# Optimization experiments

Measured on AMD Instinct MI355X. Metric: run time of the kernel, lower is better.

The kernel has to match this reference:

```python
import jax, jax.numpy as jnp
import numpy as np

N_HEADS = 8

def setup_inputs() -> dict:
    key = jax.random.key(0)
    ks = jax.random.split(key, 12)
    B, S2, C, H, W = 2, 2048, 1280, 256, 256
    s = 0.02  # weight init scale
    return {
        'hidden_states': jax.random.normal(ks[0], (B, S2, C), dtype=jnp.float32),
        'src_mask': (jax.random.uniform(ks[1], (B, 1, H, W)) > 0.5).astype(jnp.float32),
        'attn_wq': jax.random.normal(ks[2], (C, C), dtype=jnp.float32) * s,
        'attn_wk': jax.random.normal(ks[3], (C, C), dtype=jnp.float32) * s,
        'attn_wv': jax.random.normal(ks[4], (C, C), dtype=jnp.float32) * s,
        'out_w': jax.random.normal(ks[5], (C, C), dtype=jnp.float32) * s,
        'out_b': jnp.zeros((C,), dtype=jnp.float32),
        'proc_wq': jax.random.normal(ks[6], (C, C), dtype=jnp.float32) * s,
        'proc_wk': jax.random.normal(ks[7], (C, C), dtype=jnp.float32) * s,
        'proc_wv': jax.random.normal(ks[8], (C, C), dtype=jnp.float32) * s,
        'ww': jax.random.normal(ks[9], (C + 1, 1), dtype=jnp.float32) * s,
        'wb': jnp.zeros((1,), dtype=jnp.float32),
    }


def reference(hidden_states, src_mask, attn_wq, attn_wk, attn_wv, out_w, out_b,
              proc_wq, proc_wk, proc_wv, ww, wb):
    B, S2, C = hidden_states.shape
    S = S2 // 2  # condition_flag=False: sequence is two images concatenated
    _, _, H, W = src_mask.shape
    r = int(np.sqrt((H * W) / S))  # nearest-neighbor downsample ratio
    # F.interpolate(mode='nearest') with exact integer ratio == strided slice
    m = src_mask[:, 0, ::r, ::r].reshape(B, S, 1)          # [B, S, 1]
    mask = jnp.concatenate([m, m], axis=1)                 # [B, 2S, 1]
    # sigmoid gate blending the two query projections
    gate_in = jnp.concatenate([hidden_states, mask], axis=-1)  # [B, 2S, C+1]
    w = jax.nn.sigmoid(gate_in @ ww + wb)                  # [B, 2S, 1]
    query = (hidden_states @ attn_wq) * w + (hidden_states @ proc_wq) * (1.0 - w)
    # keys/values: first half through attn's projections, second half through processor's
    e1, e2 = hidden_states[:, :S], hidden_states[:, S:]
    key = jnp.concatenate([e1 @ attn_wk, e2 @ proc_wk], axis=1)
    value = jnp.concatenate([e1 @ attn_wv, e2 @ proc_wv], axis=1)
    d = C // N_HEADS
    def split_heads(x):
        return x.reshape(B, S2, N_HEADS, d).transpose(0, 2, 1, 3)  # [B, H, S2, d]
    qh, kh, vh = split_heads(query), split_heads(key), split_heads(value)
    scale = float(1.0 / np.sqrt(d))
    scores = jnp.einsum('bhqd,bhkd->bhqk', qh, kh) * scale
    probs = jax.nn.softmax(scores, axis=-1)
    out = jnp.einsum('bhqk,bhkd->bhqd', probs, vh)
    out = out.transpose(0, 2, 1, 3).reshape(B, S2, C)
    out = out @ out_w + out_b
    # residual connection, rescale_output_factor == 1
    return out + hidden_states
```

## Files before the change

### kernel.cpp

```cpp
#include <hip/hip_runtime.h>

typedef unsigned short u16;
typedef u16 u16x4 __attribute__((ext_vector_type(4)));
typedef u16 u16x8 __attribute__((ext_vector_type(8)));
typedef __bf16 bf16x8 __attribute__((ext_vector_type(8)));
typedef float f32x4 __attribute__((ext_vector_type(4)));
typedef unsigned u32x4 __attribute__((ext_vector_type(4)));

#define DEVI __device__ __forceinline__

#if __has_builtin(__builtin_amdgcn_exp2f)
#define EXP2F __builtin_amdgcn_exp2f
#else
#define EXP2F exp2f
#endif

DEVI u16 f2b(float f) {
  unsigned u = __builtin_bit_cast(unsigned, f);
  u += 0x7fffu + ((u >> 16) & 1u);
  return (u16)(u >> 16);
}

DEVI float b2f(u16 v) { return __builtin_bit_cast(float, (unsigned)v << 16); }

DEVI unsigned cvtpk_bf16(float lo, float hi) {
  unsigned r;
  asm("v_cvt_pk_bf16_f32 %0, %1, %2" : "=v"(r) : "v"(lo), "v"(hi));
  return r;
}

DEVI f32x4 mfma16(u16x8 a, u16x8 b, f32x4 c) {
  return __builtin_amdgcn_mfma_f32_16x16x32_bf16(
      __builtin_bit_cast(bf16x8, a), __builtin_bit_cast(bf16x8, b), c, 0, 0, 0);
}

DEVI void async_copy16(const u16* g, u16* l) {
  __builtin_amdgcn_global_load_lds(
      (__attribute__((address_space(1))) unsigned int*)(g),
      (__attribute__((address_space(3))) unsigned int*)(l), 16, 0, 0);
}

DEVI void fence_barrier() {
  asm volatile("" ::: "memory");
  __builtin_amdgcn_s_barrier();
  asm volatile("" ::: "memory");
}

__global__ void prep_kernel(const float* __restrict__ hs, const float* __restrict__ mask,
                            const float* __restrict__ ww, const float* __restrict__ wb,
                            u16* __restrict__ hsb, float* __restrict__ wgate) {
  int token = blockIdx.x;
  int tid = threadIdx.x;
  const float* row = hs + (size_t)token * 1280;
  u16* orow = hsb + (size_t)token * 1280;
  float acc = 0.f;
#pragma unroll
  for (int i = 0; i < 5; i++) {
    int c = i * 256 + tid;
    float v = row[c];
    orow[c] = f2b(v);
    acc += v * ww[c];
  }
#pragma unroll
  for (int off = 1; off < 64; off <<= 1) acc += __shfl_xor(acc, off);
  __shared__ float partial[4];
  int wid = tid >> 6;
  if ((tid & 63) == 0) partial[wid] = acc;
  __syncthreads();
  if (tid == 0) {
    float tot = partial[0] + partial[1] + partial[2] + partial[3];
    int b = token >> 11, t = token & 2047;
    int s = t & 1023;
    float mv = mask[b * 65536 + ((s >> 5) * 8) * 256 + (s & 31) * 8];
    float z = tot + mv * ww[1280] + wb[0];
    wgate[token] = 1.f / (1.f + __expf(-z));
  }
}

__global__ void wtrans_kernel(const float* w0, const float* w1, const float* w2,
                              const float* w3, const float* w4, const float* w5,
                              const float* w6, u16* __restrict__ out) {
  const float* src;
  switch (blockIdx.z) {
    case 0: src = w0; break; case 1: src = w1; break; case 2: src = w2; break;
    case 3: src = w3; break; case 4: src = w4; break; case 5: src = w5; break;
    default: src = w6; break;
  }
  u16* dst = out + (size_t)blockIdx.z * 1280 * 1280;
  __shared__ float tile[32][33];
  int tx = threadIdx.x & 31, ty = threadIdx.x >> 5;
  int k0 = blockIdx.x * 32, n0 = blockIdx.y * 32;
#pragma unroll
  for (int r = 0; r < 4; r++)
    tile[ty + r * 8][tx] = src[(size_t)(k0 + ty + r * 8) * 1280 + n0 + tx];
  __syncthreads();
#pragma unroll
  for (int r = 0; r < 4; r++)
    dst[(size_t)(n0 + ty + r * 8) * 1280 + k0 + tx] = f2b(tile[tx][ty + r * 8]);
}

__launch_bounds__(256, 4)
__global__ void gemm_qdual_kernel(const u16* __restrict__ A, const u16* __restrict__ Wt,
                                  const float* __restrict__ wgate, float qscale,
                                  u16* __restrict__ Qout) {
  const int K = 1280, N = 1280;
  const size_t WSZ = (size_t)1280 * 1280;
  __shared__ u16 As[128 * 32];
  __shared__ u16 Bs[64 * 32];
  __shared__ u16 Bs2[64 * 32];

  int tid = threadIdx.x;
  int wid = tid >> 6, lane = tid & 63;
  int q = lane & 15, jl = lane >> 4;
  int nb = blockIdx.x, mb = blockIdx.y, z = blockIdx.z;
  int m0 = mb * 128, n0 = nb * 128;

  const u16* B0 = Wt + 0 * WSZ;
  const u16* B1 = Wt + 4 * WSZ;

  f32x4 zero = {0.f, 0.f, 0.f, 0.f};
  f32x4 acc[4][4];
#pragma unroll
  for (int i = 0; i < 4; i++)
#pragma unroll
    for (int j = 0; j < 4; j++) acc[i][j] = zero;

  int wr = wid >> 1, wc = wid & 1;
  int brow = tid >> 2, bseg = tid & 3;

  for (int kk = 0; kk < 40; kk++) {
    int k0 = kk * 32;
#pragma unroll
    for (int i = 0; i < 2; i++) {
      int slot = i * 256 + tid;
      int row = slot >> 2, seg = slot & 3;
      async_copy16(A + (size_t)(m0 + row) * K + k0 + seg * 8, As + (size_t)(i * 256 + wid * 64) * 8);
    }
    int nrow = n0 + (z << 6) + brow;
    async_copy16(B0 + (size_t)nrow * K + k0 + bseg * 8, Bs + (size_t)tid * 8);
    async_copy16(B1 + (size_t)nrow * K + k0 + bseg * 8, Bs2 + (size_t)tid * 8);
    asm volatile("s_waitcnt vmcnt(0)" ::: "memory");
    __syncthreads();

    u16x8 af[4];
#pragma unroll
    for (int mi = 0; mi < 4; mi++)
      af[mi] = *(const u16x8*)(As + (wr * 64 + mi * 16 + q) * 32 + jl * 8);
#pragma unroll
    for (int ni = 0; ni < 2; ni++) {
      u16x8 bf0 = *(const u16x8*)(Bs + (wc * 32 + ni * 16 + q) * 32 + jl * 8);
      u16x8 bf1 = *(const u16x8*)(Bs2 + (wc * 32 + ni * 16 + q) * 32 + jl * 8);
#pragma unroll
      for (int mi = 0; mi < 4; mi++) {
        acc[mi][ni] = mfma16(af[mi], bf0, acc[mi][ni]);
        acc[mi][2 + ni] = mfma16(af[mi], bf1, acc[mi][2 + ni]);
      }
    }
    __syncthreads();
  }

#pragma unroll
  for (int mi = 0; mi < 4; mi++)
#pragma unroll
    for (int r = 0; r < 4; r++) {
      int row = m0 + wr * 64 + mi * 16 + (jl << 2) + r;
      float w = wgate[row];
#pragma unroll
      for (int ni = 0; ni < 2; ni++) {
        int col = n0 + (z << 6) + wc * 32 + ni * 16 + q;
        float v = (w * acc[mi][ni][r] + (1.f - w) * acc[mi][2 + ni][r]) * qscale;
        Qout[(size_t)row * N + col] = f2b(v);
      }
    }
}

__launch_bounds__(256, 4)
__global__ void gemm_kv_kernel(const u16* __restrict__ A, const u16* __restrict__ Wt,
                               u16* __restrict__ Kout, u16* __restrict__ VTout) {
  const int K = 1280, N = 1280;
  const size_t WSZ = (size_t)1280 * 1280;
  __shared__ u16 As[128 * 32];
  __shared__ u16 Bs[64 * 32];
  __shared__ u16 Bs2[64 * 32];

  int tid = threadIdx.x;
  int wid = tid >> 6, lane = tid & 63;
  int q = lane & 15, jl = lane >> 4;
  int nb = blockIdx.x, mb = blockIdx.y;
  bool isV = (blockIdx.z == 1);
  int m0 = mb * 128, n0 = nb * 128;
  bool first = ((m0 & 2047) < 1024);

  const u16* B0 = isV ? (first ? Wt + 2 * WSZ : Wt + 6 * WSZ)
                      : (first ? Wt + 1 * WSZ : Wt + 5 * WSZ);

  f32x4 zero = {0.f, 0.f, 0.f, 0.f};
  f32x4 acc[4][4];
#pragma unroll
  for (int i = 0; i < 4; i++)
#pragma unroll
    for (int j = 0; j < 4; j++) acc[i][j] = zero;

  int wr = wid >> 1, wc = wid & 1;
  int brow = tid >> 2, bseg = tid & 3;

  for (int kk = 0; kk < 40; kk++) {
    int k0 = kk * 32;
#pragma unroll
    for (int i = 0; i < 2; i++) {
      int slot = i * 256 + tid;
      int row = slot >> 2, seg = slot & 3;
      async_copy16(A + (size_t)(m0 + row) * K + k0 + seg * 8, As + (size_t)(i * 256 + wid * 64) * 8);
    }
    async_copy16(B0 + (size_t)(n0 + brow) * K + k0 + bseg * 8, Bs + (size_t)tid * 8);
    async_copy16(B0 + (size_t)(n0 + 64 + brow) * K + k0 + bseg * 8, Bs2 + (size_t)tid * 8);
    asm volatile("s_waitcnt vmcnt(0)" ::: "memory");
    __syncthreads();

    u16x8 af[4];
#pragma unroll
    for (int mi = 0; mi < 4; mi++)
      af[mi] = *(const u16x8*)(As + (wr * 64 + mi * 16 + q) * 32 + jl * 8);
    const u16* Bsel = wc ? Bs2 : Bs;
    u16x8 bfr[4];
#pragma unroll
    for (int ni = 0; ni < 4; ni++)
      bfr[ni] = *(const u16x8*)(Bsel + (ni * 16 + q) * 32 + jl * 8);
#pragma unroll
    for (int mi = 0; mi < 4; mi++)
#pragma unroll
      for (int ni = 0; ni < 4; ni++)
        acc[mi][ni] = mfma16(af[mi], bfr[ni], acc[mi][ni]);
    __syncthreads();
  }

  if (!isV) {
#pragma unroll
    for (int mi = 0; mi < 4; mi++)
#pragma unroll
      for (int ni = 0; ni < 4; ni++)
#pragma unroll
        for (int r = 0; r < 4; r++) {
          int row = m0 + wr * 64 + mi * 16 + (jl << 2) + r;
          int col = n0 + wc * 64 + ni * 16 + q;
          Kout[(size_t)row * N + col] = f2b(acc[mi][ni][r]);
        }
  } else {
#pragma unroll
    for (int mi = 0; mi < 4; mi++)
#pragma unroll
      for (int ni = 0; ni < 4; ni++) {
        int row0 = m0 + wr * 64 + mi * 16 + (jl << 2);
        int col = n0 + wc * 64 + ni * 16 + q;
        int b = row0 >> 11, s = row0 & 2047;
        int h = col / 160, c_in = col - h * 160;
        u16x4 v = {f2b(acc[mi][ni][0]), f2b(acc[mi][ni][1]),
                   f2b(acc[mi][ni][2]), f2b(acc[mi][ni][3])};
        *(u16x4*)(VTout + ((size_t)(b * 8 + h) * 160 + c_in) * 2048 + s) = v;
      }
  }
}

template <int SPLIT>
__launch_bounds__(256)
__global__ void flash_kernel(const u16* __restrict__ Q, const u16* __restrict__ Kg,
                             const u16* __restrict__ VTg, u16* __restrict__ O,
                             u16* __restrict__ Opart, float* __restrict__ MLbuf) {
  const int C = 1280;
  int bid = blockIdx.x;
  int qb = bid & 31, h = (bid >> 5) & 7, b = bid >> 8;
  int sp = (SPLIT > 1) ? (int)blockIdx.y : 0;
  int tid = threadIdx.x, wid = tid >> 6, lane = tid & 63;
  int q = lane & 15, jl = lane >> 4;

  int t0, NT;
  if (SPLIT == 3) { t0 = sp * 11; NT = (sp < 2) ? 11 : 10; }
  else if (SPLIT == 1) { t0 = 0; NT = 32; }
  else { t0 = sp * (32 / SPLIT); NT = 32 / SPLIT; }

  const size_t baseQ = ((size_t)(b * 2048 + qb * 64)) * C + h * 160;
  const size_t baseK = ((size_t)(b * 2048)) * C + h * 160;
  const size_t baseVT = (size_t)(b * 8 + h) * 160 * 2048;

  __shared__ u16 Ks[64 * 160];
  __shared__ u16 Vts[160 * 64];

  const u16* kbase = Kg + baseK + (size_t)(t0 * 64) * C;
  const u16* vbase = VTg + baseVT + t0 * 64;
  unsigned koff[5];
#pragma unroll
  for (int j = 0; j < 5; j++) {
    int s = (wid + 4 * j) * 64 + lane;
    int r = s / 20, cp = s - r * 20;
    int c = cp ^ ((r >> 1) & 3);
    koff[j] = (unsigned)(r * C + c * 8);
  }
  unsigned voff[5];
#pragma unroll
  for (int j = 0; j < 5; j++) {
    int gc = (wid + 4 * j) * 64 + lane;
    int c = gc >> 3, jj = gc & 7;
    voff[j] = (unsigned)(c * 2048 + ((jj ^ (c & 7)) << 3));
  }

#define STAGE_K()                                                  \
  do {                                                             \
    _Pragma("unroll") for (int j = 0; j < 5; j++)                  \
        async_copy16(kbase + koff[j], Ks + (wid + 4 * j) * 512);   \
  } while (0)
#define STAGE_V()                                                  \
  do {                                                             \
    _Pragma("unroll") for (int j = 0; j < 5; j++)                  \
        async_copy16(vbase + voff[j], Vts + (wid + 4 * j) * 512);  \
  } while (0)

  const int kro = ((jl ^ ((q >> 1) & 3)) << 3);

  const int addr0 = (q + 16 * ((jl * 2 + 0) & 3)) << 2;
  const int addr1 = (q + 16 * ((jl * 2 + 1) & 3)) << 2;
  const bool hihalf = (lane >= 32);

  u16x8 qf[5];
  {
    const u16* qrow = Q + baseQ + (size_t)(wid * 16 + q) * C;
#pragma unroll
    for (int ks = 0; ks < 5; ks++)
      qf[ks] = *(const u16x8*)(qrow + ks * 32 + jl * 8);
  }

  f32x4 zero = {0.f, 0.f, 0.f, 0.f};
  f32x4 oacc[10];
#pragma unroll
  for (int i = 0; i < 10; i++) oacc[i] = zero;
  float mrow = -1e30f, lrow = 0.f;

  STAGE_K();
  STAGE_V();

  for (int kti = 0; kti < NT; kti++) {
    bool last = (kti == NT - 1);
    asm volatile("s_waitcnt vmcnt(5)" ::: "memory");
    fence_barrier();

    f32x4 sc[4];
#pragma unroll
    for (int ct = 0; ct < 4; ct++) {
      f32x4 a = zero;
#pragma unroll
      for (int ks = 0; ks < 5; ks++) {
        u16x8 kf = *(const u16x8*)(&Ks[(ct * 16 + q) * 160 + ks * 32 + kro]);
        a = mfma16(kf, qf[ks], a);
      }
      sc[ct] = a;
    }

    fence_barrier();
    if (!last) { kbase += 64 * C; STAGE_K(); }

    float m = sc[0][0];
#pragma unroll
    for (int ct = 0; ct < 4; ct++)
#pragma unroll
      for (int r = 0; r < 4; r++) m = fmaxf(m, sc[ct][r]);
    m = fmaxf(m, __shfl_xor(m, 16));
    m = fmaxf(m, __shfl_xor(m, 32));

    if (__any(m > mrow + 8.f)) {
      float mnew = fmaxf(mrow, m);
      float alpha = EXP2F(mrow - mnew);
      mrow = mnew;
      float rs = 0.f;
#pragma unroll
      for (int ct = 0; ct < 4; ct++)
#pragma unroll
        for (int r = 0; r < 4; r++) {
          float p = EXP2F(sc[ct][r] - mnew);
          sc[ct][r] = p;
          rs += p;
        }
      lrow = lrow * alpha + rs;
#pragma unroll
      for (int ci = 0; ci < 10; ci++) oacc[ci] *= alpha;
    } else {
      float rs = 0.f;
#pragma unroll
      for (int ct = 0; ct < 4; ct++)
#pragma unroll
        for (int r = 0; r < 4; r++) {
          float p = EXP2F(sc[ct][r] - mrow);
          sc[ct][r] = p;
          rs += p;
        }
      lrow += rs;
    }

    unsigned pk0[4], pk1[4];
#pragma unroll
    for (int ct = 0; ct < 4; ct++) {
      pk0[ct] = cvtpk_bf16(sc[ct][0], sc[ct][1]);
      pk1[ct] = cvtpk_bf16(sc[ct][2], sc[ct][3]);
    }

    if (!last) { asm volatile("s_waitcnt vmcnt(5)" ::: "memory"); }
    else       { asm volatile("s_waitcnt vmcnt(0)" ::: "memory"); }
    fence_barrier();

#pragma unroll
    for (int kt2 = 0; kt2 < 2; kt2++) {
      const int cA = kt2 * 2, cB = kt2 * 2 + 1;
      int a0 = __builtin_amdgcn_ds_bpermute(addr0, (int)pk0[cA]);
      int a1 = __builtin_amdgcn_ds_bpermute(addr0, (int)pk1[cA]);
      int a2 = __builtin_amdgcn_ds_bpermute(addr1, (int)pk0[cA]);
      int a3 = __builtin_amdgcn_ds_bpermute(addr1, (int)pk1[cA]);
      int b0 = __builtin_amdgcn_ds_bpermute(addr0, (int)pk0[cB]);
      int b1 = __builtin_amdgcn_ds_bpermute(addr0, (int)pk1[cB]);
      int b2 = __builtin_amdgcn_ds_bpermute(addr1, (int)pk0[cB]);
      int b3 = __builtin_amdgcn_ds_bpermute(addr1, (int)pk1[cB]);
      u32x4 d;
      d[0] = (unsigned)(hihalf ? b0 : a0);
      d[1] = (unsigned)(hihalf ? b1 : a1);
      d[2] = (unsigned)(hihalf ? b2 : a2);
      d[3] = (unsigned)(hihalf ? b3 : a3);
      u16x8 pf = __builtin_bit_cast(u16x8, d);
#pragma unroll
      for (int ci = 0; ci < 10; ci++) {
        int c = ci * 16 + q;
        int jj = kt2 * 4 + jl;
        u16x8 vf = *(const u16x8*)(&Vts[c * 64 + ((jj ^ (c & 7)) << 3)]);
        oacc[ci] = mfma16(vf, pf, oacc[ci]);
      }
    }

    fence_barrier();
    if (!last) { vbase += 64; STAGE_V(); }
  }
#undef STAGE_K
#undef STAGE_V

  lrow += __shfl_xor(lrow, 16);
  lrow += __shfl_xor(lrow, 32);
  float linv = 1.f / lrow;

  int qrow = qb * 64 + wid * 16 + q;
  if constexpr (SPLIT > 1) {
    size_t g0 = (size_t)sp * 4096 + (size_t)b * 2048 + qrow;
#pragma unroll
    for (int ci = 0; ci < 10; ci++) {
      int col = h * 160 + ci * 16 + (jl << 2);
      u16x4 v = {f2b(oacc[ci][0] * linv), f2b(oacc[ci][1] * linv),
                 f2b(oacc[ci][2] * linv), f2b(oacc[ci][3] * linv)};
      *(u16x4*)(Opart + g0 * 1280 + col) = v;
    }
    if (lane < 16) {
      size_t mi = (g0 * 8 + h) * 2;
      MLbuf[mi] = mrow;
      MLbuf[mi + 1] = lrow;
    }
  } else {
#pragma unroll
    for (int ci = 0; ci < 10; ci++) {
      int col = h * 160 + ci * 16 + (jl << 2);
      u16x4 v = {f2b(oacc[ci][0] * linv), f2b(oacc[ci][1] * linv),
                 f2b(oacc[ci][2] * linv), f2b(oacc[ci][3] * linv)};
      *(u16x4*)(O + ((size_t)(b * 2048) + qrow) * C + col) = v;
    }
  }
}

__global__ void combine_kernel(const u16* __restrict__ Opart, const float* __restrict__ MLbuf,
                               u16* __restrict__ O) {
  int idx = blockIdx.x * 256 + threadIdx.x;
  int token = idx / 160;
  int h = (idx - token * 160) / 20;
  size_t i0 = ((size_t)token * 8 + h) * 2;
  const size_t MLP = (size_t)4096 * 16;
  float m0 = MLbuf[i0], l0 = MLbuf[i0 + 1];
  float m1 = MLbuf[i0 + MLP], l1 = MLbuf[i0 + MLP + 1];
  float m2 = MLbuf[i0 + 2 * MLP], l2 = MLbuf[i0 + 2 * MLP + 1];
  float m = fmaxf(fmaxf(m0, m1), m2);
  float w0 = EXP2F(m0 - m) * l0, w1 = EXP2F(m1 - m) * l1, w2 = EXP2F(m2 - m) * l2;
  float inv = 1.f / (w0 + w1 + w2);
  w0 *= inv; w1 *= inv; w2 *= inv;
  const size_t OPP = (size_t)655360;
  u16x8 a = *(const u16x8*)(Opart + (size_t)idx * 8);
  u16x8 c = *(const u16x8*)(Opart + (OPP + idx) * 8);
  u16x8 d = *(const u16x8*)(Opart + (2 * OPP + idx) * 8);
  u16x8 o;
#pragma unroll
  for (int j = 0; j < 8; j++)
    o[j] = f2b(b2f(a[j]) * w0 + b2f(c[j]) * w1 + b2f(d[j]) * w2);
  *(u16x8*)(O + (size_t)idx * 8) = o;
}

__launch_bounds__(256)
__global__ void gemm_out_kernel(const u16* __restrict__ A, const u16* __restrict__ Bt,
                                float* __restrict__ Cf, const float* __restrict__ bias,
                                const float* __restrict__ resid) {
  const int K = 1280, N = 1280;
  __shared__ u16 As[128 * 32];
  __shared__ u16 Bs[128 * 32];

  int tid = threadIdx.x;
  int wid = tid >> 6, lane = tid & 63;
  int nb = blockIdx.x, mb = blockIdx.y;
  int m0 = mb * 128, n0 = nb * 128;

  f32x4 zero = {0.f, 0.f, 0.f, 0.f};
  f32x4 acc[4][4];
#pragma unroll
  for (int i = 0; i < 4; i++)
#pragma unroll
    for (int j = 0; j < 4; j++) acc[i][j] = zero;

  int wr = wid >> 1, wc = wid & 1;

  for (int kk = 0; kk < 40; kk++) {
    int k0 = kk * 32;
#pragma unroll
    for (int i = 0; i < 2; i++) {
      int slot = i * 256 + tid;
      int row = slot >> 2, seg = slot & 3;
      async_copy16(A + (size_t)(m0 + row) * K + k0 + seg * 8, As + (size_t)(i * 256 + wid * 64) * 8);
      async_copy16(Bt + (size_t)(n0 + row) * K + k0 + seg * 8, Bs + (size_t)(i * 256 + wid * 64) * 8);
    }
    asm volatile("s_waitcnt vmcnt(0)" ::: "memory");
    __syncthreads();

    u16x8 af[4], bfr[4];
#pragma unroll
    for (int mi = 0; mi < 4; mi++)
      af[mi] = *(const u16x8*)(As + (wr * 64 + mi * 16 + (lane & 15)) * 32 + (lane >> 4) * 8);
#pragma unroll
    for (int ni = 0; ni < 4; ni++)
      bfr[ni] = *(const u16x8*)(Bs + (wc * 64 + ni * 16 + (lane & 15)) * 32 + (lane >> 4) * 8);
#pragma unroll
    for (int mi = 0; mi < 4; mi++)
#pragma unroll
      for (int ni = 0; ni < 4; ni++)
        acc[mi][ni] = mfma16(af[mi], bfr[ni], acc[mi][ni]);
    __syncthreads();
  }

#pragma unroll
  for (int mi = 0; mi < 4; mi++)
#pragma unroll
    for (int ni = 0; ni < 4; ni++)
#pragma unroll
      for (int r = 0; r < 4; r++) {
        int row = m0 + wr * 64 + mi * 16 + ((lane >> 4) << 2) + r;
        int col = n0 + wc * 64 + ni * 16 + (lane & 15);
        Cf[(size_t)row * N + col] = acc[mi][ni][r] + bias[col] + resid[(size_t)row * N + col];
      }
}

extern "C" void kernel_launch(void* const* d_in, const int* in_sizes, int n_in,
                              void* d_out, int out_size, void* d_ws, size_t ws_size,
                              hipStream_t stream) {
  const float* hs      = (const float*)d_in[0];
  const float* mask    = (const float*)d_in[1];
  const float* attn_wq = (const float*)d_in[2];
  const float* attn_wk = (const float*)d_in[3];
  const float* attn_wv = (const float*)d_in[4];
  const float* out_w   = (const float*)d_in[5];
  const float* out_b   = (const float*)d_in[6];
  const float* proc_wq = (const float*)d_in[7];
  const float* proc_wk = (const float*)d_in[8];
  const float* proc_wv = (const float*)d_in[9];
  const float* ww      = (const float*)d_in[10];
  const float* wb      = (const float*)d_in[11];
  float* out = (float*)d_out;

  char* ws = (char*)d_ws;
  const size_t TOK = (size_t)4096 * 1280;
  u16* hsb = (u16*)(ws);
  u16* Qb  = (u16*)(ws + 2 * TOK);
  u16* Kb  = (u16*)(ws + 4 * TOK);
  u16* VTb = (u16*)(ws + 6 * TOK);
  u16* AOb = (u16*)(ws + 8 * TOK);
  u16* Wt  = (u16*)(ws + 10 * TOK);
  float* wgate = (float*)(ws + 10 * TOK + (size_t)7 * 1280 * 1280 * 2);
  char* extra = ws + 10 * TOK + (size_t)7 * 1280 * 1280 * 2 + 16384;
  u16* Opart = (u16*)extra;
  float* MLbuf = (float*)(extra + (size_t)3 * 4096 * 1280 * 2);
  size_t need = (size_t)(extra - ws) + (size_t)3 * 4096 * 1280 * 2 + (size_t)3 * 4096 * 8 * 8;

  prep_kernel<<<4096, 256, 0, stream>>>(hs, mask, ww, wb, hsb, wgate);
  wtrans_kernel<<<dim3(40, 40, 7), 256, 0, stream>>>(attn_wq, attn_wk, attn_wv, out_w,
                                                     proc_wq, proc_wk, proc_wv, Wt);
  const size_t WSZ = (size_t)1280 * 1280;
  const float qscale = 0.11405505533858971f;
  gemm_qdual_kernel<<<dim3(10, 32, 2), 256, 0, stream>>>(hsb, Wt, wgate, qscale, Qb);
  gemm_kv_kernel<<<dim3(10, 32, 2), 256, 0, stream>>>(hsb, Wt, Kb, VTb);

  if (ws_size >= need) {
    flash_kernel<3><<<dim3(512, 3), 256, 0, stream>>>(Qb, Kb, VTb, nullptr, Opart, MLbuf);
    combine_kernel<<<2560, 256, 0, stream>>>(Opart, MLbuf, AOb);
  } else {
    flash_kernel<1><<<dim3(512, 1), 256, 0, stream>>>(Qb, Kb, VTb, AOb, nullptr, nullptr);
  }
  gemm_out_kernel<<<dim3(10, 32), 256, 0, stream>>>(AOb, Wt + 3 * WSZ, out, out_b, hs);
}
```

Baseline: 232.0 us.

## Double-buffer GEMM LDS stages and restructure flash attention into 512-thread blocks

All three projection/output GEMMs now use double-buffered shared-memory tiles, prefetching the next K-slice while computing the current one, with partial vmcnt waits to hide global load latency. The flash kernel moves to 512-thread blocks covering 128 query rows, with four waves loading K tiles and four loading V tiles so each staging is split by role. The KV split changes from 3 to 2, and the combine kernel is updated to merge two partials. This trades doubled LDS use and lower occupancy for better latency hiding and K/V reuse across more queries.

```diff
diff --git a/kernel.cpp b/kernel.cpp
--- a/kernel.cpp
+++ b/kernel.cpp
@@ -105,9 +105,9 @@
                                   u16* __restrict__ Qout) {
   const int K = 1280, N = 1280;
   const size_t WSZ = (size_t)1280 * 1280;
-  __shared__ u16 As[128 * 32];
-  __shared__ u16 Bs[64 * 32];
-  __shared__ u16 Bs2[64 * 32];
+  __shared__ u16 As[2][128 * 32];
+  __shared__ u16 Bs[2][64 * 32];
+  __shared__ u16 Bs2[2][64 * 32];
 
   int tid = threadIdx.x;
   int wid = tid >> 6, lane = tid & 63;
@@ -127,37 +127,49 @@
 
   int wr = wid >> 1, wc = wid & 1;
   int brow = tid >> 2, bseg = tid & 3;
-
+  int nrow = n0 + (z << 6) + brow;
+
+#define QSTAGE(buf, kk)                                                           \
+  do {                                                                            \
+    int k0 = (kk) * 32;                                                           \
+    _Pragma("unroll") for (int i = 0; i < 2; i++) {                               \
+      int slot = i * 256 + tid;                                                   \
+      int row = slot >> 2, seg = slot & 3;                                        \
+      async_copy16(A + (size_t)(m0 + row) * K + k0 + seg * 8,                     \
+                   As[buf] + (size_t)(i * 256 + wid * 64) * 8);                   \
+    }                                                                             \
+    async_copy16(B0 + (size_t)nrow * K + k0 + bseg * 8, Bs[buf] + (size_t)tid * 8);   \
+    async_copy16(B1 + (size_t)nrow * K + k0 + bseg * 8, Bs2[buf] + (size_t)tid * 8);  \
+  } while (0)
+
+  QSTAGE(0, 0);
   for (int kk = 0; kk < 40; kk++) {
-    int k0 = kk * 32;
-#pragma unroll
-    for (int i = 0; i < 2; i++) {
-      int slot = i * 256 + tid;
-      int row = slot >> 2, seg = slot & 3;
-      async_copy16(A + (size_t)(m0 + row) * K + k0 + seg * 8, As + (size_t)(i * 256 + wid * 64) * 8);
-    }
-    int nrow = n0 + (z << 6) + brow;
-    async_copy16(B0 + (size_t)nrow * K + k0 + bseg * 8, Bs + (size_t)tid * 8);
-    async_copy16(B1 + (size_t)nrow * K + k0 + bseg * 8, Bs2 + (size_t)tid * 8);
-    asm volatile("s_waitcnt vmcnt(0)" ::: "memory");
-    __syncthreads();
+    int cur = kk & 1;
+    if (kk < 39) {
+      QSTAGE(cur ^ 1, kk + 1);
+      asm volatile("s_waitcnt vmcnt(4)" ::: "memory");
+    } else {
+      asm volatile("s_waitcnt vmcnt(0)" ::: "memory");
+    }
+    fence_barrier();
 
     u16x8 af[4];
 #pragma unroll
     for (int mi = 0; mi < 4; mi++)
-      af[mi] = *(const u16x8*)(As + (wr * 64 + mi * 16 + q) * 32 + jl * 8);
+      af[mi] = *(const u16x8*)(As[cur] + (wr * 64 + mi * 16 + q) * 32 + jl * 8);
 #pragma unroll
     for (int ni = 0; ni < 2; ni++) {
-      u16x8 bf0 = *(const u16x8*)(Bs + (wc * 32 + ni * 16 + q) * 32 + jl * 8);
-      u16x8 bf1 = *(const u16x8*)(Bs2 + (wc * 32 + ni * 16 + q) * 32 + jl * 8);
+      u16x8 bf0 = *(const u16x8*)(Bs[cur] + (wc * 32 + ni * 16 + q) * 32 + jl * 8);
+      u16x8 bf1 = *(const u16x8*)(Bs2[cur] + (wc * 32 + ni * 16 + q) * 32 + jl * 8);
 #pragma unroll
       for (int mi = 0; mi < 4; mi++) {
         acc[mi][ni] = mfma16(af[mi], bf0, acc[mi][ni]);
         acc[mi][2 + ni] = mfma16(af[mi], bf1, acc[mi][2 + ni]);
       }
     }
-    __syncthreads();
-  }
+    fence_barrier();
+  }
+#undef QSTAGE
 
 #pragma unroll
   for (int mi = 0; mi < 4; mi++)
@@ -179,9 +191,9 @@
                                u16* __restrict__ Kout, u16* __restrict__ VTout) {
   const int K = 1280, N = 1280;
   const size_t WSZ = (size_t)1280 * 1280;
-  __shared__ u16 As[128 * 32];
-  __shared__ u16 Bs[64 * 32];
-  __shared__ u16 Bs2[64 * 32];
+  __shared__ u16 As[2][128 * 32];
+  __shared__ u16 Bs[2][64 * 32];
+  __shared__ u16 Bs2[2][64 * 32];
 
   int tid = threadIdx.x;
   int wid = tid >> 6, lane = tid & 63;
@@ -204,24 +216,35 @@
   int wr = wid >> 1, wc = wid & 1;
   int brow = tid >> 2, bseg = tid & 3;
 
+#define KVSTAGE(buf, kk)                                                          \
+  do {                                                                            \
+    int k0 = (kk) * 32;                                                           \
+    _Pragma("unroll") for (int i = 0; i < 2; i++) {                               \
+      int slot = i * 256 + tid;                                                   \
+      int row = slot >> 2, seg = slot & 3;                                        \
+      async_copy16(A + (size_t)(m0 + row) * K + k0 + seg * 8,                     \
+                   As[buf] + (size_t)(i * 256 + wid * 64) * 8);                   \
+    }                                                                             \
+    async_copy16(B0 + (size_t)(n0 + brow) * K + k0 + bseg * 8, Bs[buf] + (size_t)tid * 8);       \
+    async_copy16(B0 + (size_t)(n0 + 64 + brow) * K + k0 + bseg * 8, Bs2[buf] + (size_t)tid * 8); \
+  } while (0)
+
+  KVSTAGE(0, 0);
   for (int kk = 0; kk < 40; kk++) {
-    int k0 = kk * 32;
-#pragma unroll
-    for (int i = 0; i < 2; i++) {
-      int slot = i * 256 + tid;
-      int row = slot >> 2, seg = slot & 3;
-      async_copy16(A + (size_t)(m0 + row) * K + k0 + seg * 8, As + (size_t)(i * 256 + wid * 64) * 8);
-    }
-    async_copy16(B0 + (size_t)(n0 + brow) * K + k0 + bseg * 8, Bs + (size_t)tid * 8);
-    async_copy16(B0 + (size_t)(n0 + 64 + brow) * K + k0 + bseg * 8, Bs2 + (size_t)tid * 8);
-    asm volatile("s_waitcnt vmcnt(0)" ::: "memory");
-    __syncthreads();
+    int cur = kk & 1;
+    if (kk < 39) {
+      KVSTAGE(cur ^ 1, kk + 1);
+      asm volatile("s_waitcnt vmcnt(4)" ::: "memory");
+    } else {
+      asm volatile("s_waitcnt vmcnt(0)" ::: "memory");
+    }
+    fence_barrier();
 
     u16x8 af[4];
 #pragma unroll
     for (int mi = 0; mi < 4; mi++)
-      af[mi] = *(const u16x8*)(As + (wr * 64 + mi * 16 + q) * 32 + jl * 8);
-    const u16* Bsel = wc ? Bs2 : Bs;
+      af[mi] = *(const u16x8*)(As[cur] + (wr * 64 + mi * 16 + q) * 32 + jl * 8);
+    const u16* Bsel = wc ? Bs2[cur] : Bs[cur];
     u16x8 bfr[4];
 #pragma unroll
     for (int ni = 0; ni < 4; ni++)
@@ -231,8 +254,9 @@
 #pragma unroll
       for (int ni = 0; ni < 4; ni++)
         acc[mi][ni] = mfma16(af[mi], bfr[ni], acc[mi][ni]);
-    __syncthreads();
-  }
+    fence_barrier();
+  }
+#undef KVSTAGE
 
   if (!isV) {
 #pragma unroll
@@ -262,56 +286,60 @@
 }
 
 template <int SPLIT>
-__launch_bounds__(256)
+__launch_bounds__(512)
 __global__ void flash_kernel(const u16* __restrict__ Q, const u16* __restrict__ Kg,
                              const u16* __restrict__ VTg, u16* __restrict__ O,
                              u16* __restrict__ Opart, float* __restrict__ MLbuf) {
   const int C = 1280;
   int bid = blockIdx.x;
-  int qb = bid & 31, h = (bid >> 5) & 7, b = bid >> 8;
+  int qb = bid & 15, h = (bid >> 4) & 7, b = bid >> 7;
   int sp = (SPLIT > 1) ? (int)blockIdx.y : 0;
   int tid = threadIdx.x, wid = tid >> 6, lane = tid & 63;
   int q = lane & 15, jl = lane >> 4;
 
-  int t0, NT;
-  if (SPLIT == 3) { t0 = sp * 11; NT = (sp < 2) ? 11 : 10; }
-  else if (SPLIT == 1) { t0 = 0; NT = 32; }
-  else { t0 = sp * (32 / SPLIT); NT = 32 / SPLIT; }
-
-  const size_t baseQ = ((size_t)(b * 2048 + qb * 64)) * C + h * 160;
+  const int NT = 32 / SPLIT;
+  const int t0 = sp * NT;
+
+  const size_t baseQ = ((size_t)(b * 2048 + qb * 128)) * C + h * 160;
   const size_t baseK = ((size_t)(b * 2048)) * C + h * 160;
   const size_t baseVT = (size_t)(b * 8 + h) * 160 * 2048;
 
   __shared__ u16 Ks[64 * 160];
   __shared__ u16 Vts[160 * 64];
 
-  const u16* kbase = Kg + baseK + (size_t)(t0 * 64) * C;
-  const u16* vbase = VTg + baseVT + t0 * 64;
-  unsigned koff[5];
-#pragma unroll
-  for (int j = 0; j < 5; j++) {
-    int s = (wid + 4 * j) * 64 + lane;
-    int r = s / 20, cp = s - r * 20;
-    int c = cp ^ ((r >> 1) & 3);
-    koff[j] = (unsigned)(r * C + c * 8);
-  }
-  unsigned voff[5];
-#pragma unroll
-  for (int j = 0; j < 5; j++) {
-    int gc = (wid + 4 * j) * 64 + lane;
-    int c = gc >> 3, jj = gc & 7;
-    voff[j] = (unsigned)(c * 2048 + ((jj ^ (c & 7)) << 3));
-  }
-
-#define STAGE_K()                                                  \
+  const bool isK = (wid < 4);
+  int sw = wid & 3;
+  const u16* sbase;
+  u16* sdst;
+  size_t sadv;
+  unsigned soff[5];
+  if (isK) {
+    sbase = Kg + baseK + (size_t)(t0 * 64) * C;
+    sdst = Ks;
+    sadv = (size_t)64 * C;
+#pragma unroll
+    for (int j = 0; j < 5; j++) {
+      int s = (sw + 4 * j) * 64 + lane;
+      int r = s / 20, cp = s - r * 20;
+      int c = cp ^ ((r >> 1) & 3);
+      soff[j] = (unsigned)(r * C + c * 8);
+    }
+  } else {
+    sbase = VTg + baseVT + t0 * 64;
+    sdst = Vts;
+    sadv = 64;
+#pragma unroll
+    for (int j = 0; j < 5; j++) {
+      int gc = (sw + 4 * j) * 64 + lane;
+      int c = gc >> 3, jj = gc & 7;
+      soff[j] = (unsigned)(c * 2048 + ((jj ^ (c & 7)) << 3));
+    }
+  }
+
+#define STAGE5()                                                   \
   do {                                                             \
     _Pragma("unroll") for (int j = 0; j < 5; j++)                  \
-        async_copy16(kbase + koff[j], Ks + (wid + 4 * j) * 512);   \
-  } while (0)
-#define STAGE_V()                                                  \
-  do {                                                             \
-    _Pragma("unroll") for (int j = 0; j < 5; j++)                  \
-        async_copy16(vbase + voff[j], Vts + (wid + 4 * j) * 512);  \
+        async_copy16(sbase + soff[j], sdst + (sw + 4 * j) * 512);  \
   } while (0)
 
   const int kro = ((jl ^ ((q >> 1) & 3)) << 3);
@@ -334,12 +362,11 @@
   for (int i = 0; i < 10; i++) oacc[i] = zero;
   float mrow = -1e30f, lrow = 0.f;
 
-  STAGE_K();
-  STAGE_V();
+  STAGE5();
 
   for (int kti = 0; kti < NT; kti++) {
     bool last = (kti == NT - 1);
-    asm volatile("s_waitcnt vmcnt(5)" ::: "memory");
+    if (isK) { asm volatile("s_waitcnt vmcnt(0)" ::: "memory"); }
     fence_barrier();
 
     f32x4 sc[4];
@@ -355,7 +382,7 @@
     }
 
     fence_barrier();
-    if (!last) { kbase += 64 * C; STAGE_K(); }
+    if (isK && !last) { sbase += sadv; STAGE5(); }
 
     float m = sc[0][0];
 #pragma unroll
@@ -401,8 +428,7 @@
       pk1[ct] = cvtpk_bf16(sc[ct][2], sc[ct][3]);
     }
 
-    if (!last) { asm volatile("s_waitcnt vmcnt(5)" ::: "memory"); }
-    else       { asm volatile("s_waitcnt vmcnt(0)" ::: "memory"); }
+    if (!isK) { asm volatile("s_waitcnt vmcnt(0)" ::: "memory"); }
     fence_barrier();
 
 #pragma unroll
@@ -432,16 +458,15 @@
     }
 
     fence_barrier();
-    if (!last) { vbase += 64; STAGE_V(); }
-  }
-#undef STAGE_K
-#undef STAGE_V
+    if (!isK && !last) { sbase += sadv; STAGE5(); }
+  }
+#undef STAGE5
 
   lrow += __shfl_xor(lrow, 16);
   lrow += __shfl_xor(lrow, 32);
   float linv = 1.f / lrow;
 
-  int qrow = qb * 64 + wid * 16 + q;
+  int qrow = qb * 128 + wid * 16 + q;
   if constexpr (SPLIT > 1) {
     size_t g0 = (size_t)sp * 4096 + (size_t)b * 2048 + qrow;
 #pragma unroll
@@ -476,29 +501,27 @@
   const size_t MLP = (size_t)4096 * 16;
   float m0 = MLbuf[i0], l0 = MLbuf[i0 + 1];
   float m1 = MLbuf[i0 + MLP], l1 = MLbuf[i0 + MLP + 1];
-  float m2 = MLbuf[i0 + 2 * MLP], l2 = MLbuf[i0 + 2 * MLP + 1];
-  float m = fmaxf(fmaxf(m0, m1), m2);
-  float w0 = EXP2F(m0 - m) * l0, w1 = EXP2F(m1 - m) * l1, w2 = EXP2F(m2 - m) * l2;
-  float inv = 1.f / (w0 + w1 + w2);
-  w0 *= inv; w1 *= inv; w2 *= inv;
+  float m = fmaxf(m0, m1);
+  float w0 = EXP2F(m0 - m) * l0, w1 = EXP2F(m1 - m) * l1;
+  float inv = 1.f / (w0 + w1);
+  w0 *= inv; w1 *= inv;
   const size_t OPP = (size_t)655360;
   u16x8 a = *(const u16x8*)(Opart + (size_t)idx * 8);
   u16x8 c = *(const u16x8*)(Opart + (OPP + idx) * 8);
-  u16x8 d = *(const u16x8*)(Opart + (2 * OPP + idx) * 8);
   u16x8 o;
 #pragma unroll
   for (int j = 0; j < 8; j++)
-    o[j] = f2b(b2f(a[j]) * w0 + b2f(c[j]) * w1 + b2f(d[j]) * w2);
+    o[j] = f2b(b2f(a[j]) * w0 + b2f(c[j]) * w1);
   *(u16x8*)(O + (size_t)idx * 8) = o;
 }
 
-__launch_bounds__(256)
+__launch_bounds__(256, 4)
 __global__ void gemm_out_kernel(const u16* __restrict__ A, const u16* __restrict__ Bt,
                                 float* __restrict__ Cf, const float* __restrict__ bias,
                                 const float* __restrict__ resid) {
   const int K = 1280, N = 1280;
-  __shared__ u16 As[128 * 32];
-  __shared__ u16 Bs[128 * 32];
+  __shared__ u16 As[2][128 * 32];
+  __shared__ u16 Bs[2][128 * 32];
 
   int tid = threadIdx.x;
   int wid = tid >> 6, lane = tid & 63;
@@ -514,32 +537,45 @@
 
   int wr = wid >> 1, wc = wid & 1;
 
+#define OSTAGE(buf, kk)                                                           \
+  do {                                                                            \
+    int k0 = (kk) * 32;                                                           \
+    _Pragma("unroll") for (int i = 0; i < 2; i++) {                               \
+      int slot = i * 256 + tid;                                                   \
+      int row = slot >> 2, seg = slot & 3;                                        \
+      async_copy16(A + (size_t)(m0 + row) * K + k0 + seg * 8,                     \
+                   As[buf] + (size_t)(i * 256 + wid * 64) * 8);                   \
+      async_copy16(Bt + (size_t)(n0 + row) * K + k0 + seg * 8,                    \
+                   Bs[buf] + (size_t)(i * 256 + wid * 64) * 8);                   \
+    }                                                                             \
+  } while (0)
+
+  OSTAGE(0, 0);
   for (int kk = 0; kk < 40; kk++) {
-    int k0 = kk * 32;
-#pragma unroll
-    for (int i = 0; i < 2; i++) {
-      int slot = i * 256 + tid;
-      int row = slot >> 2, seg = slot & 3;
-      async_copy16(A + (size_t)(m0 + row) * K + k0 + seg * 8, As + (size_t)(i * 256 + wid * 64) * 8);
-      async_copy16(Bt + (size_t)(n0 + row) * K + k0 + seg * 8, Bs + (size_t)(i * 256 + wid * 64) * 8);
-    }
-    asm volatile("s_waitcnt vmcnt(0)" ::: "memory");
-    __syncthreads();
+    int cur = kk & 1;
+    if (kk < 39) {
+      OSTAGE(cur ^ 1, kk + 1);
+      asm volatile("s_waitcnt vmcnt(4)" ::: "memory");
+    } else {
+      asm volatile("s_waitcnt vmcnt(0)" ::: "memory");
+    }
+    fence_barrier();
 
     u16x8 af[4], bfr[4];
 #pragma unroll
     for (int mi = 0; mi < 4; mi++)
-      af[mi] = *(const u16x8*)(As + (wr * 64 + mi * 16 + (lane & 15)) * 32 + (lane >> 4) * 8);
+      af[mi] = *(const u16x8*)(As[cur] + (wr * 64 + mi * 16 + (lane & 15)) * 32 + (lane >> 4) * 8);
 #pragma unroll
     for (int ni = 0; ni < 4; ni++)
-      bfr[ni] = *(const u16x8*)(Bs + (wc * 64 + ni * 16 + (lane & 15)) * 32 + (lane >> 4) * 8);
+      bfr[ni] = *(const u16x8*)(Bs[cur] + (wc * 64 + ni * 16 + (lane & 15)) * 32 + (lane >> 4) * 8);
 #pragma unroll
     for (int mi = 0; mi < 4; mi++)
 #pragma unroll
       for (int ni = 0; ni < 4; ni++)
         acc[mi][ni] = mfma16(af[mi], bfr[ni], acc[mi][ni]);
-    __syncthreads();
-  }
+    fence_barrier();
+  }
+#undef OSTAGE
 
 #pragma unroll
   for (int mi = 0; mi < 4; mi++)
@@ -581,8 +617,8 @@
   float* wgate = (float*)(ws + 10 * TOK + (size_t)7 * 1280 * 1280 * 2);
   char* extra = ws + 10 * TOK + (size_t)7 * 1280 * 1280 * 2 + 16384;
   u16* Opart = (u16*)extra;
-  float* MLbuf = (float*)(extra + (size_t)3 * 4096 * 1280 * 2);
-  size_t need = (size_t)(extra - ws) + (size_t)3 * 4096 * 1280 * 2 + (size_t)3 * 4096 * 8 * 8;
+  float* MLbuf = (float*)(extra + (size_t)2 * 4096 * 1280 * 2);
+  size_t need = (size_t)(extra - ws) + (size_t)2 * 4096 * 1280 * 2 + (size_t)2 * 4096 * 8 * 8;
 
   prep_kernel<<<4096, 256, 0, stream>>>(hs, mask, ww, wb, hsb, wgate);
   wtrans_kernel<<<dim3(40, 40, 7), 256, 0, stream>>>(attn_wq, attn_wk, attn_wv, out_w,
@@ -593,10 +629,10 @@
   gemm_kv_kernel<<<dim3(10, 32, 2), 256, 0, stream>>>(hsb, Wt, Kb, VTb);
 
   if (ws_size >= need) {
-    flash_kernel<3><<<dim3(512, 3), 256, 0, stream>>>(Qb, Kb, VTb, nullptr, Opart, MLbuf);
+    flash_kernel<2><<<dim3(256, 2), 512, 0, stream>>>(Qb, Kb, VTb, nullptr, Opart, MLbuf);
     combine_kernel<<<2560, 256, 0, stream>>>(Opart, MLbuf, AOb);
   } else {
-    flash_kernel<1><<<dim3(512, 1), 256, 0, stream>>>(Qb, Kb, VTb, AOb, nullptr, nullptr);
+    flash_kernel<1><<<dim3(256, 1), 512, 0, stream>>>(Qb, Kb, VTb, AOb, nullptr, nullptr);
   }
   gemm_out_kernel<<<dim3(10, 32), 256, 0, stream>>>(AOb, Wt + 3 * WSZ, out, out_b, hs);
 }
```

Result: faster. 224.9 us (-3.1%).
